# Kernel tuning notes

Hardware: AMD Instinct MI355X
Metric: run time of the kernel (lower is better)

Reference implementation:

```python
import jax, jax.numpy as jnp
import numpy as np

R_MIN = 0.01
R_MAX = 0.6
H = 32            # polar radial bins (after pooling)
W = 64            # polar angular bins (after pooling)
UP_R = 10         # radial upsampling factor
UP_T = 10         # angular upsampling factor
ATT_ALPHA = 5.0
B, C, IMG = 64, 3, 224


def _conv(x, w, b):
    # NCHW valid conv, stride 1 (matches nn.Conv2d default padding=0)
    y = jax.lax.conv_general_dilated(x, w, (1, 1), 'VALID',
                                     dimension_numbers=('NCHW', 'OIHW', 'NCHW'))
    return y + b[None, :, None, None]


def _maxpool2(x):
    return jax.lax.reduce_window(x, -jnp.inf, jax.lax.max,
                                 (1, 1, 2, 2), (1, 1, 2, 2), 'VALID')


def _grid_sample_border(x, grid):
    # F.grid_sample, bilinear, padding_mode='border', align_corners=False
    Bn, Cn, Hi, Wi = x.shape
    ix = ((grid[..., 0] + 1.0) * Wi - 1.0) * 0.5   # x-coord -> width index
    iy = ((grid[..., 1] + 1.0) * Hi - 1.0) * 0.5   # y-coord -> height index
    x0f = jnp.floor(ix)
    y0f = jnp.floor(iy)
    wx = (ix - x0f)[..., None]
    wy = (iy - y0f)[..., None]
    x0 = jnp.clip(x0f.astype(jnp.int32), 0, Wi - 1)
    x1 = jnp.clip(x0f.astype(jnp.int32) + 1, 0, Wi - 1)
    y0 = jnp.clip(y0f.astype(jnp.int32), 0, Hi - 1)
    y1 = jnp.clip(y0f.astype(jnp.int32) + 1, 0, Hi - 1)
    bidx = jnp.arange(Bn)[:, None, None]
    v00 = x[bidx, :, y0, x0]   # [B,Hg,Wg,C]
    v01 = x[bidx, :, y0, x1]
    v10 = x[bidx, :, y1, x0]
    v11 = x[bidx, :, y1, x1]
    out = (v00 * (1 - wx) * (1 - wy) + v01 * wx * (1 - wy)
           + v10 * (1 - wx) * wy + v11 * wx * wy)
    return jnp.transpose(out, (0, 3, 1, 2))  # [B,C,Hg,Wg]


def setup_inputs() -> dict:
    key = jax.random.key(0)
    ks = jax.random.split(key, 10)
    x = jax.random.normal(ks[0], (B, C, IMG, IMG), dtype=jnp.float32)
    l_t_prev = jax.random.uniform(ks[1], (B, 2), dtype=jnp.float32)
    conv1_w = jax.random.normal(ks[2], (6, C, 5, 5), dtype=jnp.float32) * 0.1
    conv1_b = jnp.zeros((6,), jnp.float32)
    conv2_w = jax.random.normal(ks[3], (16, 6, 5, 5), dtype=jnp.float32) * 0.1
    conv2_b = jnp.zeros((16,), jnp.float32)
    fc1_w = jax.random.normal(ks[4], (8, 16), dtype=jnp.float32) * 0.1
    fc1_b = jnp.zeros((8,), jnp.float32)
    fc2_w = jax.random.normal(ks[5], (2, 8), dtype=jnp.float32) * 0.1
    fc2_b = jnp.zeros((2,), jnp.float32)
    return dict(x=x, l_t_prev=l_t_prev, conv1_w=conv1_w, conv1_b=conv1_b,
                conv2_w=conv2_w, conv2_b=conv2_b, fc1_w=fc1_w, fc1_b=fc1_b,
                fc2_w=fc2_w, fc2_b=fc2_b)


def reference(x, l_t_prev, conv1_w, conv1_b, conv2_w, conv2_b,
              fc1_w, fc1_b, fc2_w, fc2_b):
    # --- attention branch: conv -> maxpool -> conv -> GAP -> fc -> sigmoid ---
    h = _conv(x, conv1_w, conv1_b)
    h = _maxpool2(h)
    h = _conv(h, conv2_w, conv2_b)
    feat = h.mean(axis=(2, 3))                     # AdaptiveAvgPool2d(1), [B,16]
    h = jax.nn.relu(feat @ fc1_w.T + fc1_b)
    weight = jax.nn.sigmoid(h @ fc2_w.T + fc2_b) * ATT_ALPHA   # [B,2]
    # --- per-batch log-polar grid ---
    Hg, Wg = H * UP_R, W * UP_T
    angle = 2.0 * jnp.pi * jnp.arange(Wg, dtype=jnp.float32) / Wg
    unit = jnp.stack([jnp.sin(angle), jnp.cos(angle)], axis=-1)   # [Wg,2]
    start = jnp.log(R_MIN * weight[:, 0])
    stop = jnp.log(R_MAX * weight[:, 1])
    t = jnp.arange(Hg, dtype=jnp.float32) / (Hg - 1)
    radii = jnp.exp(start[:, None] + (stop - start)[:, None] * t[None])  # [B,Hg]
    grid = radii[:, :, None, None] * unit[None, None]     # [B,Hg,Wg,2]
    grid = grid + l_t_prev[:, None, None, :]
    # --- irregular bilinear sampling + box filter ---
    sampled = _grid_sample_border(x, grid)                 # [B,C,Hg,Wg]
    Bn, Cn = sampled.shape[:2]
    pooled = sampled.reshape(Bn, Cn, H, UP_R, W, UP_T).mean(axis=(3, 5))
    return pooled, weight
```

## Files before the change

### kernel.cpp

```cpp
#include <hip/hip_runtime.h>
#include <math.h>

#define Bn    64
#define Cn    3
#define IMG   224
#define PLANE (IMG*IMG)
#define C1    6
#define P1    110
#define NVALID (106*106)
#define Hh    32
#define Ww    64
#define UPR   10
#define UPT   10
#define Hg    (Hh*UPR)
#define Wg    (Ww*UPT)
#define POOLED_SIZE (Bn*Cn*Hh*Ww)
#define NCHUNK 28
#define PSTRIDE 152
#define ROWB  (IMG*8)
#define TPB1  448

typedef unsigned short u16;
typedef unsigned long long ull;
typedef _Float16 h8v __attribute__((ext_vector_type(8)));
typedef float f4v __attribute__((ext_vector_type(4)));

#define PART_FLOATS ((size_t)Bn * NCHUNK * PSTRIDE)
#define X4B_U16     ((size_t)Bn * PLANE * 4)
#define WS_NEEDED   ((PART_FLOATS + Bn * 2) * 4 + X4B_U16 * 2)

__device__ __forceinline__ unsigned hpack(float a, float b) {
    union { _Float16 h; u16 u; } x, y;
    x.h = (_Float16)a; y.h = (_Float16)b;
    return (unsigned)x.u | ((unsigned)y.u << 16);
}
__device__ __forceinline__ float h2lo(unsigned v) {
    union { _Float16 h; u16 u; } c; c.u = (u16)(v & 0xffffu); return (float)c.h;
}
__device__ __forceinline__ float h2hi(unsigned v) {
    union { _Float16 h; u16 u; } c; c.u = (u16)(v >> 16); return (float)c.h;
}

#define GSHFL(v, idx) __shfl((v), (lane & 48) + (idx), 64)

__global__ __launch_bounds__(TPB1) void k1_fused(
    const float* __restrict__ x,
    const float* __restrict__ w1,
    const float* __restrict__ b1,
    float* __restrict__ partial,
    u16* __restrict__ x4h,
    int do_pack)
{
    __shared__ __attribute__((aligned(16))) unsigned char xs[12 * ROWB + 128];
    __shared__ __attribute__((aligned(16))) _Float16 sa[5][64][8];
    __shared__ float rowR[7][C1][4];
    __shared__ float edgeLo[4][C1][4];
    __shared__ float edgeHi[4][C1][4];

    const int b     = blockIdx.x;
    const int chunk = blockIdx.y;
    const int tid   = threadIdx.x;
    const int wid   = tid >> 6;
    const int lane  = tid & 63;
    const int n     = lane & 15;
    const int g     = lane >> 4;
    const int gy0   = chunk * 8;

    const float* xb = x + (size_t)b * (Cn * PLANE);
    u16* ob = x4h + (size_t)b * PLANE * 4;

    if (wid == 0) {
        #pragma unroll
        for (int ky = 0; ky < 5; ++ky) {
            #pragma unroll
            for (int j = 0; j < 8; ++j) {
                const int kmem = g * 8 + j;
                const int ic = kmem & 3, kx = kmem >> 2;
                float w = 0.0f;
                if (n < C1 && ic < 3 && kx < 5)
                    w = w1[((n * 3 + ic) * 5 + ky) * 5 + kx];
                sa[ky][lane][j] = (_Float16)w;
            }
        }
    } else {
        for (int i = tid - 64; i < 12 * 112; i += TPB1 - 64) {
            const int r = i / 112;
            const int p = i - r * 112;
            const int gy = gy0 + r;
            uint4 U; U.x = U.y = U.z = U.w = 0u;
            if (gy < IMG) {
                const float2 v0 = *(const float2*)(xb + 0 * PLANE + gy * IMG + 2 * p);
                const float2 v1 = *(const float2*)(xb + 1 * PLANE + gy * IMG + 2 * p);
                const float2 v2 = *(const float2*)(xb + 2 * PLANE + gy * IMG + 2 * p);
                U.x = hpack(v0.x, v1.x);
                U.y = hpack(v2.x, 0.0f);
                U.z = hpack(v0.y, v1.y);
                U.w = hpack(v2.y, 0.0f);
            }
            *(uint4*)(xs + r * ROWB + p * 16) = U;
            if (do_pack && r < 8)
                *(uint4*)(ob + ((size_t)gy * IMG + 2 * p) * 4) = U;
        }
    }
    __syncthreads();

    h8v a[5];
    #pragma unroll
    for (int ky = 0; ky < 5; ++ky) a[ky] = *(const h8v*)&sa[ky][lane][0];
    f4v binit;
    #pragma unroll
    for (int e = 0; e < 4; ++e) {
        const int oc = g * 4 + e;
        binit[e] = (oc < C1) ? b1[oc] : 0.0f;
    }

    float colsum[4][4];
    #pragma unroll
    for (int py = 0; py < 4; ++py)
        #pragma unroll
        for (int e = 0; e < 4; ++e) colsum[py][e] = 0.0f;

    #pragma unroll
    for (int si = 0; si < 2; ++si) {
        const int s = wid * 2 + si;
        const unsigned sByte = (unsigned)(s * 128 + n * 8 + g * 16);

        f4v acc[8];
        #pragma unroll
        for (int q = 0; q < 8; ++q) acc[q] = binit;

        #pragma unroll
        for (int r = 0; r < 12; ++r) {
            h8v bf;
            const unsigned char* bp = xs + r * ROWB + sByte;
            ((ull*)&bf)[0] = *(const ull*)bp;
            ((ull*)&bf)[1] = *(const ull*)(bp + 8);
            #pragma unroll
            for (int ky = 0; ky < 5; ++ky) {
                const int q = r - ky;
                if (q >= 0 && q < 8)
                    acc[q] = __builtin_amdgcn_mfma_f32_16x16x32_f16(
                        a[ky], bf, acc[q], 0, 0, 0);
            }
        }

        #pragma unroll
        for (int py = 0; py < 4; ++py) {
            #pragma unroll
            for (int e = 0; e < 4; ++e) {
                float t = fmaxf(acc[2 * py][e], acc[2 * py + 1][e]);
                t = fmaxf(t, __shfl_xor(t, 1, 64));
                if (s == 13 && n >= 12) t = 0.0f;
                colsum[py][e] += t;
                const int oc = g * 4 + e;
                if (s == 0) {
                    const float c0 = GSHFL(t, 0), c1 = GSHFL(t, 2);
                    const float c2 = GSHFL(t, 4), c3 = GSHFL(t, 6);
                    const float S1 = c0, S2 = S1 + c1, S3 = S2 + c2, S4 = S3 + c3;
                    const float sv = (n == 0) ? S1 : (n == 1) ? S2 : (n == 2) ? S3 : S4;
                    if (n < 4 && oc < C1) edgeLo[py][oc][n] = sv;
                }
                if (s == 13) {
                    const float d109 = GSHFL(t, 10), d108 = GSHFL(t, 8);
                    const float d107 = GSHFL(t, 6),  d106 = GSHFL(t, 4);
                    const float U1 = d109, U2 = U1 + d108, U3 = U2 + d107, U4 = U3 + d106;
                    const float uv = (n == 0) ? U1 : (n == 1) ? U2 : (n == 2) ? U3 : U4;
                    if (n < 4 && oc < C1) edgeHi[py][oc][n] = uv;
                }
            }
        }
    }

    #pragma unroll
    for (int py = 0; py < 4; ++py) {
        #pragma unroll
        for (int e = 0; e < 4; ++e) {
            float v = colsum[py][e];
            v += __shfl_xor(v, 2, 64);
            v += __shfl_xor(v, 4, 64);
            v += __shfl_xor(v, 8, 64);
            const int oc = g * 4 + e;
            if (n == 0 && oc < C1) rowR[wid][oc][py] = v;
        }
    }
    __syncthreads();

    if (tid < 150) {
        const int oc = tid / 25;
        const int rem = tid - oc * 25;
        const int ky = rem / 5, kx = rem - ky * 5;
        float total = 0.0f;
        #pragma unroll
        for (int py = 0; py < 4; ++py) {
            const int y = chunk * 4 + py;
            const bool valid = (y < P1) && ((unsigned)(y - ky) <= 105u);
            float v = rowR[0][oc][py] + rowR[1][oc][py] + rowR[2][oc][py]
                    + rowR[3][oc][py] + rowR[4][oc][py] + rowR[5][oc][py]
                    + rowR[6][oc][py];
            if (kx > 0) v -= edgeLo[py][oc][kx - 1];
            if (kx < 4) v -= edgeHi[py][oc][3 - kx];
            total += valid ? v : 0.0f;
        }
        partial[((size_t)b * NCHUNK + chunk) * PSTRIDE + tid] = total;
    }
}

__global__ __launch_bounds__(256) void k2_head(
    const float* __restrict__ partial, const float* __restrict__ w2,
    const float* __restrict__ b2, const float* __restrict__ fc1w,
    const float* __restrict__ fc1b, const float* __restrict__ fc2w,
    const float* __restrict__ fc2b, float* __restrict__ wt_ws,
    float* __restrict__ out)
{
    const int b = blockIdx.x;
    const int tid = threadIdx.x;
    __shared__ float wsb[150];
    __shared__ float sfeat[16];
    __shared__ float sh[8];

    if (tid < 150) {
        const float* p = partial + (size_t)b * NCHUNK * PSTRIDE + tid;
        float s = 0.0f;
        #pragma unroll
        for (int c = 0; c < NCHUNK; ++c) s += p[c * PSTRIDE];
        wsb[tid] = s;
    }
    __syncthreads();
    if (tid < 16) {
        float s = 0.0f;
        for (int j = 0; j < 150; ++j) s += w2[tid * 150 + j] * wsb[j];
        sfeat[tid] = b2[tid] + s * (1.0f / (float)NVALID);
    }
    __syncthreads();
    if (tid < 8) {
        float s = fc1b[tid];
        #pragma unroll
        for (int j = 0; j < 16; ++j) s += fc1w[tid * 16 + j] * sfeat[j];
        sh[tid] = fmaxf(s, 0.0f);
    }
    __syncthreads();
    if (tid < 2) {
        float s = fc2b[tid];
        #pragma unroll
        for (int j = 0; j < 8; ++j) s += fc2w[tid * 8 + j] * sh[j];
        float sig = (s >= 0.0f) ? (1.0f / (1.0f + expf(-s)))
                                : (expf(s) / (1.0f + expf(s)));
        const float wgt = 5.0f * sig;
        wt_ws[b * 2 + tid] = wgt;
        out[POOLED_SIZE + b * 2 + tid] = wgt;
    }
}

__device__ __forceinline__ void sample_coords(
    float gxn, float gyn, int& x0, int& y0, float& wx, float& wy)
{
    float ix = ((gxn + 1.0f) * (float)IMG - 1.0f) * 0.5f;
    float iy = ((gyn + 1.0f) * (float)IMG - 1.0f) * 0.5f;
    ix = fminf(fmaxf(ix, 0.0f), (float)(IMG - 1));
    iy = fminf(fmaxf(iy, 0.0f), (float)(IMG - 1));
    x0 = (int)ix; if (x0 > IMG - 2) x0 = IMG - 2;
    y0 = (int)iy; if (y0 > IMG - 2) y0 = IMG - 2;
    wx = ix - (float)x0;
    wy = iy - (float)y0;
}

__global__ __launch_bounds__(640) void k3_sample_pool_f16(
    const u16* __restrict__ x4h,
    const float* __restrict__ ltp,
    const float* __restrict__ wt,
    float* __restrict__ out)
{
    __shared__ float part[3 * Wg];

    const int L = blockIdx.x;
    const int q = L >> 3;
    const int h = q & 31;
    const int b = (L & 7) + 8 * (q >> 5);
    const int tid = threadIdx.x;

    const float w0 = wt[b * 2 + 0];
    const float w1 = wt[b * 2 + 1];
    const float l0 = ltp[b * 2 + 0];
    const float l1 = ltp[b * 2 + 1];
    const float start = logf(0.01f * w0);
    const float stop  = logf(0.6f  * w1);
    const float dr = stop - start;

    const float angle = 6.283185307179586f * (float)tid / (float)Wg;
    const float sn = __sinf(angle);
    const float cs = __cosf(angle);

    const u16* xb4 = x4h + (size_t)b * PLANE * 4;

    int xi[UPR], yi[UPR];
    float wxa[UPR], wya[UPR];
    #pragma unroll
    for (int i = 0; i < UPR; ++i) {
        const float ri = __expf(start + dr * ((float)(h * UPR + i)
                                              * (1.0f / (float)(Hg - 1))));
        sample_coords(ri * sn + l0, ri * cs + l1, xi[i], yi[i], wxa[i], wya[i]);
    }

    float acc0 = 0.0f, acc1 = 0.0f, acc2 = 0.0f;
    #pragma unroll
    for (int bb = 0; bb < 2; ++bb) {
        uint4 R0[5], R1[5];
        #pragma unroll
        for (int i = 0; i < 5; ++i) {
            const int s = bb * 5 + i;
            const u16* base = xb4 + ((size_t)(yi[s] * IMG + xi[s])) * 4;
            R0[i] = *(const uint4*)(base);
            R1[i] = *(const uint4*)(base + IMG * 4);
        }
        #pragma unroll
        for (int i = 0; i < 5; ++i) {
            const int s = bb * 5 + i;
            const float wx = wxa[s], wy = wya[s];
            const float wx0 = 1.0f - wx, wy0 = 1.0f - wy;
            const float w00 = wx0 * wy0, w01 = wx * wy0;
            const float w10 = wx0 * wy,  w11 = wx * wy;
            acc0 += w00*h2lo(R0[i].x) + w01*h2lo(R0[i].z)
                  + w10*h2lo(R1[i].x) + w11*h2lo(R1[i].z);
            acc1 += w00*h2hi(R0[i].x) + w01*h2hi(R0[i].z)
                  + w10*h2hi(R1[i].x) + w11*h2hi(R1[i].z);
            acc2 += w00*h2lo(R0[i].y) + w01*h2lo(R0[i].w)
                  + w10*h2lo(R1[i].y) + w11*h2lo(R1[i].w);
        }
    }
    part[0 * Wg + tid] = acc0;
    part[1 * Wg + tid] = acc1;
    part[2 * Wg + tid] = acc2;
    __syncthreads();

    if (tid < Cn * Ww) {
        const int c = tid / Ww;
        const int w = tid % Ww;
        const float* p = part + c * Wg + w * UPT;
        float s = 0.0f;
        #pragma unroll
        for (int j = 0; j < UPT; ++j) s += p[j];
        out[(((size_t)b * Cn + c) * Hh + h) * Ww + w] = s * (1.0f / (UPR * UPT));
    }
}

__global__ __launch_bounds__(640) void k3_sample_pool_nchw(
    const float* __restrict__ x, const float* __restrict__ ltp,
    const float* __restrict__ wt, float* __restrict__ out)
{
    __shared__ float part[3 * Wg];
    const int L = blockIdx.x;
    const int q = L >> 3;
    const int h = q & 31;
    const int b = (L & 7) + 8 * (q >> 5);
    const int tid = threadIdx.x;

    const float w0 = wt[b * 2 + 0];
    const float w1 = wt[b * 2 + 1];
    const float l0 = ltp[b * 2 + 0];
    const float l1 = ltp[b * 2 + 1];
    const float start = logf(0.01f * w0);
    const float stop  = logf(0.6f  * w1);
    const float dr = stop - start;
    const float angle = 6.283185307179586f * (float)tid / (float)Wg;
    const float sn = __sinf(angle);
    const float cs = __cosf(angle);
    const float* xb = x + (size_t)b * Cn * PLANE;

    float acc0 = 0.0f, acc1 = 0.0f, acc2 = 0.0f;
    #pragma unroll
    for (int i = 0; i < UPR; ++i) {
        const float ri = __expf(start + dr * ((float)(h * UPR + i)
                                              * (1.0f / (float)(Hg - 1))));
        int x0, y0; float wx, wy;
        sample_coords(ri * sn + l0, ri * cs + l1, x0, y0, wx, wy);
        const float wx0 = 1.0f - wx, wy0 = 1.0f - wy;
        const float w00 = wx0 * wy0, w01 = wx * wy0;
        const float w10 = wx0 * wy,  w11 = wx * wy;
        const int o00 = y0 * IMG + x0;
        acc0 += w00*xb[o00] + w01*xb[o00+1] + w10*xb[o00+IMG] + w11*xb[o00+IMG+1];
        const float* x1p = xb + PLANE;
        acc1 += w00*x1p[o00] + w01*x1p[o00+1] + w10*x1p[o00+IMG] + w11*x1p[o00+IMG+1];
        const float* x2p = xb + 2 * PLANE;
        acc2 += w00*x2p[o00] + w01*x2p[o00+1] + w10*x2p[o00+IMG] + w11*x2p[o00+IMG+1];
    }
    part[0 * Wg + tid] = acc0;
    part[1 * Wg + tid] = acc1;
    part[2 * Wg + tid] = acc2;
    __syncthreads();

    if (tid < Cn * Ww) {
        const int c = tid / Ww;
        const int w = tid % Ww;
        const float* p = part + c * Wg + w * UPT;
        float s = 0.0f;
        #pragma unroll
        for (int j = 0; j < UPT; ++j) s += p[j];
        out[(((size_t)b * Cn + c) * Hh + h) * Ww + w] = s * (1.0f / (UPR * UPT));
    }
}

extern "C" void kernel_launch(void* const* d_in, const int* in_sizes, int n_in,
                              void* d_out, int out_size, void* d_ws, size_t ws_size,
                              hipStream_t stream) {
    const float* x       = (const float*)d_in[0];
    const float* ltp     = (const float*)d_in[1];
    const float* conv1_w = (const float*)d_in[2];
    const float* conv1_b = (const float*)d_in[3];
    const float* conv2_w = (const float*)d_in[4];
    const float* conv2_b = (const float*)d_in[5];
    const float* fc1_w   = (const float*)d_in[6];
    const float* fc1_b   = (const float*)d_in[7];
    const float* fc2_w   = (const float*)d_in[8];
    const float* fc2_b   = (const float*)d_in[9];
    float* out = (float*)d_out;

    const int do_pack = (ws_size >= WS_NEEDED) ? 1 : 0;

    float* part_ws = (float*)d_ws;
    float* wt_ws   = part_ws + PART_FLOATS;
    u16*   x4h     = (u16*)(wt_ws + Bn * 2);

    k1_fused<<<dim3(Bn, NCHUNK), dim3(TPB1), 0, stream>>>(
        x, conv1_w, conv1_b, part_ws, x4h, do_pack);
    k2_head<<<dim3(Bn), dim3(256), 0, stream>>>(part_ws, conv2_w, conv2_b,
                                                fc1_w, fc1_b, fc2_w, fc2_b,
                                                wt_ws, out);
    if (do_pack)
        k3_sample_pool_f16<<<dim3(Hh * Bn), dim3(Wg), 0, stream>>>(x4h, ltp, wt_ws, out);
    else
        k3_sample_pool_nchw<<<dim3(Hh * Bn), dim3(Wg), 0, stream>>>(x, ltp, wt_ws, out);
}
```

Baseline: 173.3 us.

## Drop packed fp16 image copy and sample directly from NCHW input

The conv kernel no longer writes a packed fp16 4-channel copy of the image to workspace, and the sampling kernel now reads the original fp32 NCHW planes directly, issuing batched per-channel gathers with precomputed offsets. This removes the extra global write of the packed image (about 25 MB) and the fp16 rounding of sampled values. The cost is that each sample now needs three separate per-channel gathers instead of one 16-byte load per corner.

```diff
diff --git a/kernel.cpp b/kernel.cpp
--- a/kernel.cpp
+++ b/kernel.cpp
@@ -26,20 +26,12 @@
 typedef float f4v __attribute__((ext_vector_type(4)));
 
 #define PART_FLOATS ((size_t)Bn * NCHUNK * PSTRIDE)
-#define X4B_U16     ((size_t)Bn * PLANE * 4)
-#define WS_NEEDED   ((PART_FLOATS + Bn * 2) * 4 + X4B_U16 * 2)
 
 __device__ __forceinline__ unsigned hpack(float a, float b) {
     union { _Float16 h; u16 u; } x, y;
     x.h = (_Float16)a; y.h = (_Float16)b;
     return (unsigned)x.u | ((unsigned)y.u << 16);
 }
-__device__ __forceinline__ float h2lo(unsigned v) {
-    union { _Float16 h; u16 u; } c; c.u = (u16)(v & 0xffffu); return (float)c.h;
-}
-__device__ __forceinline__ float h2hi(unsigned v) {
-    union { _Float16 h; u16 u; } c; c.u = (u16)(v >> 16); return (float)c.h;
-}
 
 #define GSHFL(v, idx) __shfl((v), (lane & 48) + (idx), 64)
 
@@ -47,9 +39,7 @@
     const float* __restrict__ x,
     const float* __restrict__ w1,
     const float* __restrict__ b1,
-    float* __restrict__ partial,
-    u16* __restrict__ x4h,
-    int do_pack)
+    float* __restrict__ partial)
 {
     __shared__ __attribute__((aligned(16))) unsigned char xs[12 * ROWB + 128];
     __shared__ __attribute__((aligned(16))) _Float16 sa[5][64][8];
@@ -67,7 +57,6 @@
     const int gy0   = chunk * 8;
 
     const float* xb = x + (size_t)b * (Cn * PLANE);
-    u16* ob = x4h + (size_t)b * PLANE * 4;
 
     if (wid == 0) {
         #pragma unroll
@@ -98,8 +87,6 @@
                 U.w = hpack(v2.y, 0.0f);
             }
             *(uint4*)(xs + r * ROWB + p * 16) = U;
-            if (do_pack && r < 8)
-                *(uint4*)(ob + ((size_t)gy * IMG + 2 * p) * 4) = U;
         }
     }
     __syncthreads();
@@ -264,8 +251,8 @@
     wy = iy - (float)y0;
 }
 
-__global__ __launch_bounds__(640) void k3_sample_pool_f16(
-    const u16* __restrict__ x4h,
+__global__ __launch_bounds__(640) void k3_sample_pool(
+    const float* __restrict__ x,
     const float* __restrict__ ltp,
     const float* __restrict__ wt,
     float* __restrict__ out)
@@ -290,102 +277,49 @@
     const float sn = __sinf(angle);
     const float cs = __cosf(angle);
 
-    const u16* xb4 = x4h + (size_t)b * PLANE * 4;
-
-    int xi[UPR], yi[UPR];
+    const float* xb = x + (size_t)b * Cn * PLANE;
+
+    int off[UPR];
     float wxa[UPR], wya[UPR];
     #pragma unroll
     for (int i = 0; i < UPR; ++i) {
         const float ri = __expf(start + dr * ((float)(h * UPR + i)
                                               * (1.0f / (float)(Hg - 1))));
-        sample_coords(ri * sn + l0, ri * cs + l1, xi[i], yi[i], wxa[i], wya[i]);
-    }
-
-    float acc0 = 0.0f, acc1 = 0.0f, acc2 = 0.0f;
-    #pragma unroll
-    for (int bb = 0; bb < 2; ++bb) {
-        uint4 R0[5], R1[5];
-        #pragma unroll
-        for (int i = 0; i < 5; ++i) {
-            const int s = bb * 5 + i;
-            const u16* base = xb4 + ((size_t)(yi[s] * IMG + xi[s])) * 4;
-            R0[i] = *(const uint4*)(base);
-            R1[i] = *(const uint4*)(base + IMG * 4);
-        }
-        #pragma unroll
-        for (int i = 0; i < 5; ++i) {
-            const int s = bb * 5 + i;
-            const float wx = wxa[s], wy = wya[s];
-            const float wx0 = 1.0f - wx, wy0 = 1.0f - wy;
-            const float w00 = wx0 * wy0, w01 = wx * wy0;
-            const float w10 = wx0 * wy,  w11 = wx * wy;
-            acc0 += w00*h2lo(R0[i].x) + w01*h2lo(R0[i].z)
-                  + w10*h2lo(R1[i].x) + w11*h2lo(R1[i].z);
-            acc1 += w00*h2hi(R0[i].x) + w01*h2hi(R0[i].z)
-                  + w10*h2hi(R1[i].x) + w11*h2hi(R1[i].z);
-            acc2 += w00*h2lo(R0[i].y) + w01*h2lo(R0[i].w)
-                  + w10*h2lo(R1[i].y) + w11*h2lo(R1[i].w);
-        }
-    }
-    part[0 * Wg + tid] = acc0;
-    part[1 * Wg + tid] = acc1;
-    part[2 * Wg + tid] = acc2;
-    __syncthreads();
-
-    if (tid < Cn * Ww) {
-        const int c = tid / Ww;
-        const int w = tid % Ww;
-        const float* p = part + c * Wg + w * UPT;
-        float s = 0.0f;
-        #pragma unroll
-        for (int j = 0; j < UPT; ++j) s += p[j];
-        out[(((size_t)b * Cn + c) * Hh + h) * Ww + w] = s * (1.0f / (UPR * UPT));
-    }
-}
-
-__global__ __launch_bounds__(640) void k3_sample_pool_nchw(
-    const float* __restrict__ x, const float* __restrict__ ltp,
-    const float* __restrict__ wt, float* __restrict__ out)
-{
-    __shared__ float part[3 * Wg];
-    const int L = blockIdx.x;
-    const int q = L >> 3;
-    const int h = q & 31;
-    const int b = (L & 7) + 8 * (q >> 5);
-    const int tid = threadIdx.x;
-
-    const float w0 = wt[b * 2 + 0];
-    const float w1 = wt[b * 2 + 1];
-    const float l0 = ltp[b * 2 + 0];
-    const float l1 = ltp[b * 2 + 1];
-    const float start = logf(0.01f * w0);
-    const float stop  = logf(0.6f  * w1);
-    const float dr = stop - start;
-    const float angle = 6.283185307179586f * (float)tid / (float)Wg;
-    const float sn = __sinf(angle);
-    const float cs = __cosf(angle);
-    const float* xb = x + (size_t)b * Cn * PLANE;
-
-    float acc0 = 0.0f, acc1 = 0.0f, acc2 = 0.0f;
-    #pragma unroll
-    for (int i = 0; i < UPR; ++i) {
-        const float ri = __expf(start + dr * ((float)(h * UPR + i)
-                                              * (1.0f / (float)(Hg - 1))));
-        int x0, y0; float wx, wy;
-        sample_coords(ri * sn + l0, ri * cs + l1, x0, y0, wx, wy);
-        const float wx0 = 1.0f - wx, wy0 = 1.0f - wy;
-        const float w00 = wx0 * wy0, w01 = wx * wy0;
-        const float w10 = wx0 * wy,  w11 = wx * wy;
-        const int o00 = y0 * IMG + x0;
-        acc0 += w00*xb[o00] + w01*xb[o00+1] + w10*xb[o00+IMG] + w11*xb[o00+IMG+1];
-        const float* x1p = xb + PLANE;
-        acc1 += w00*x1p[o00] + w01*x1p[o00+1] + w10*x1p[o00+IMG] + w11*x1p[o00+IMG+1];
-        const float* x2p = xb + 2 * PLANE;
-        acc2 += w00*x2p[o00] + w01*x2p[o00+1] + w10*x2p[o00+IMG] + w11*x2p[o00+IMG+1];
-    }
-    part[0 * Wg + tid] = acc0;
-    part[1 * Wg + tid] = acc1;
-    part[2 * Wg + tid] = acc2;
+        int x0, y0;
+        sample_coords(ri * sn + l0, ri * cs + l1, x0, y0, wxa[i], wya[i]);
+        off[i] = y0 * IMG + x0;
+    }
+
+    float accc[3];
+    #pragma unroll
+    for (int c = 0; c < 3; ++c) {
+        const float* xp = xb + c * PLANE;
+        float acc = 0.0f;
+        #pragma unroll
+        for (int bb = 0; bb < 2; ++bb) {
+            float v00[5], v01[5], v10[5], v11[5];
+            #pragma unroll
+            for (int i = 0; i < 5; ++i) {
+                const int o = off[bb * 5 + i];
+                v00[i] = xp[o];
+                v01[i] = xp[o + 1];
+                v10[i] = xp[o + IMG];
+                v11[i] = xp[o + IMG + 1];
+            }
+            #pragma unroll
+            for (int i = 0; i < 5; ++i) {
+                const int s = bb * 5 + i;
+                const float wx = wxa[s], wy = wya[s];
+                const float wx0 = 1.0f - wx, wy0 = 1.0f - wy;
+                acc += (wx0 * wy0) * v00[i] + (wx * wy0) * v01[i]
+                     + (wx0 * wy)  * v10[i] + (wx * wy)  * v11[i];
+            }
+        }
+        accc[c] = acc;
+    }
+    part[0 * Wg + tid] = accc[0];
+    part[1 * Wg + tid] = accc[1];
+    part[2 * Wg + tid] = accc[2];
     __syncthreads();
 
     if (tid < Cn * Ww) {
@@ -414,19 +348,13 @@
     const float* fc2_b   = (const float*)d_in[9];
     float* out = (float*)d_out;
 
-    const int do_pack = (ws_size >= WS_NEEDED) ? 1 : 0;
-
     float* part_ws = (float*)d_ws;
     float* wt_ws   = part_ws + PART_FLOATS;
-    u16*   x4h     = (u16*)(wt_ws + Bn * 2);
 
     k1_fused<<<dim3(Bn, NCHUNK), dim3(TPB1), 0, stream>>>(
-        x, conv1_w, conv1_b, part_ws, x4h, do_pack);
+        x, conv1_w, conv1_b, part_ws);
     k2_head<<<dim3(Bn), dim3(256), 0, stream>>>(part_ws, conv2_w, conv2_b,
                                                 fc1_w, fc1_b, fc2_w, fc2_b,
                                                 wt_ws, out);
-    if (do_pack)
-        k3_sample_pool_f16<<<dim3(Hh * Bn), dim3(Wg), 0, stream>>>(x4h, ltp, wt_ws, out);
-    else
-        k3_sample_pool_nchw<<<dim3(Hh * Bn), dim3(Wg), 0, stream>>>(x, ltp, wt_ws, out);
-}
+    k3_sample_pool<<<dim3(Hh * Bn), dim3(Wg), 0, stream>>>(x, ltp, wt_ws, out);
+}
```

Result: slower. 213.5 us (+23.2%).
